# Kernel optimization log

Hardware: AMD Instinct MI355X
Metric: run time of the kernel (lower is better)

The kernel has to match this reference:

```python
import jax, jax.numpy as jnp
import numpy as np

TOP_K = 8  # num_experts_per_tok
NEG_INF = -1e9


def setup_inputs() -> dict:
    key = jax.random.key(0)
    ks = jax.random.split(key, 6)
    B, S, H, I, E, G, GS = 1, 2048, 2048, 1408, 64, 8, 8
    sc = 0.02
    return {
        "hidden_states": jax.random.normal(ks[0], (B, S, H), jnp.float32),
        "gate_w": jax.random.normal(ks[1], (E, H), jnp.float32) * sc,
        "mask_up_w": jax.random.normal(ks[2], (G, H, GS), jnp.float32) * sc,
        "gate_proj_w": jax.random.normal(ks[3], (G, I, H), jnp.float32) * sc,
        "up_proj_w": jax.random.normal(ks[4], (G, I, H), jnp.float32) * sc,
        "down_proj_w": jax.random.normal(ks[5], (G, H, I), jnp.float32) * sc,
        "inv_map": jnp.arange(G * GS, dtype=jnp.int64).reshape(G, GS),
    }


def reference(hidden_states, gate_w, mask_up_w, gate_proj_w, up_proj_w, down_proj_w, inv_map):
    B, S, H = hidden_states.shape
    x = hidden_states.reshape(-1, H)  # [N, H]
    N = x.shape[0]
    E = gate_w.shape[0]

    # Gate: softmax scores -> top-k routing (DeepSeek-style MoEGate)
    scores = jax.nn.softmax(x @ gate_w.T, axis=-1)          # [N, E]
    topk_w, topk_idx = jax.lax.top_k(scores, TOP_K)         # [N, K]

    # Per-expert routing weight: w_e[t, e] = sum_k topk_w[t,k] * (topk_idx[t,k]==e)
    w_e = jnp.zeros((N, E), x.dtype).at[jnp.arange(N)[:, None], topk_idx].add(topk_w)

    # Gather group-local weights: flat[t, g, i] for sub-expert i of group g
    flat = w_e[:, inv_map]                                   # [N, G, GS]
    scalar = flat.sum(-1)                                    # [N, G]
    soft = jax.nn.softmax(jnp.where(flat == 0, NEG_INF, flat), axis=-1)  # [N, G, GS]

    # Mask injection: x' = x + mask_up_proj(soft)
    xg = x[:, None, :] + jnp.einsum('ngi,ghi->ngh', soft, mask_up_w)     # [N, G, H]

    # SwiGLU per group
    g = jnp.einsum('ngh,gih->ngi', xg, gate_proj_w)          # [N, G, I]
    u = jnp.einsum('ngh,gih->ngi', xg, up_proj_w)            # [N, G, I]
    a = jax.nn.silu(g) * u
    d = jnp.einsum('ngi,ghi->ngh', a, down_proj_w)           # [N, G, H]

    # scalar * output, accumulated over groups (scalar==0 rows contribute 0,
    # matching the original's zero-masked scatter)
    y = jnp.einsum('ng,ngh->nh', scalar, d)
    return y.reshape(B, S, H)
```

## Files before the change

### kernel.cpp

```cpp
#include <hip/hip_runtime.h>

#define N_TOK 2048
#define H_DIM 2048
#define I_DIM 1408
#define E_EXP 64
#define G_GRP 8
#define KTOT  (G_GRP * I_DIM)
#define NQ    (G_GRP * I_DIM * H_DIM / 4)
#define NQB   (NQ / 256)

typedef __bf16 bf16x8 __attribute__((ext_vector_type(8)));
typedef float f32x4 __attribute__((ext_vector_type(4)));

__device__ __forceinline__ unsigned short f2bf(float f) {
    unsigned int u = __builtin_bit_cast(unsigned int, f);
    u += 0x7fffu + ((u >> 16) & 1u);
    return (unsigned short)(u >> 16);
}

__device__ __forceinline__ void gl_lds16(const void* g, void* l) {
    __builtin_amdgcn_global_load_lds(
        (const __attribute__((address_space(1))) unsigned int*)g,
        (__attribute__((address_space(3))) unsigned int*)l, 16, 0, 0);
}

__device__ __forceinline__ bf16x8 lds_frag(const unsigned short* sm, int row, int c) {
    return *(const bf16x8*)&sm[(row * 8 + (c ^ (row & 7))) * 8];
}

__device__ __forceinline__ bf16x8 frag32(const unsigned short* sm, int region, int row, int q) {
    return *(const bf16x8*)&sm[(region + row * 4 + (q ^ (row & 3))) * 8];
}

__global__ __launch_bounds__(256) void k_prep(const float* __restrict__ gw,
                                              const float* __restrict__ wgp,
                                              const float* __restrict__ wup,
                                              const float* __restrict__ wdp,
                                              float* __restrict__ gwT,
                                              unsigned short* __restrict__ wgB,
                                              unsigned short* __restrict__ wuB,
                                              unsigned short* __restrict__ wdB) {
    int b = blockIdx.x, t = threadIdx.x;
    if (b < 2 * NQB) {
        const float* in = (b < NQB) ? wgp : wup;
        unsigned short* out = (b < NQB) ? wgB : wuB;
        int i = (b < NQB ? b : b - NQB) * 256 + t;
        float4 v = ((const float4*)in)[i];
        ushort4 o;
        o.x = f2bf(v.x); o.y = f2bf(v.y); o.z = f2bf(v.z); o.w = f2bf(v.w);
        ((ushort4*)out)[i] = o;
    } else if (b < 3 * NQB) {
        int idx = (b - 2 * NQB) * 256 + t;
        int i4 = idx % (I_DIM / 4);
        int h  = (idx / (I_DIM / 4)) & (H_DIM - 1);
        int g  = idx / ((I_DIM / 4) * H_DIM);
        float4 v = ((const float4*)(wdp + ((size_t)g * H_DIM + h) * I_DIM))[i4];
        ushort4 o;
        o.x = f2bf(v.x); o.y = f2bf(v.y); o.z = f2bf(v.z); o.w = f2bf(v.w);
        ((ushort4*)(wdB + ((size_t)h * G_GRP + g) * I_DIM))[i4] = o;
    } else {
        int i = (b - 3 * NQB) * 256 + t;
        gwT[i] = gw[(i & 63) * H_DIM + (i >> 6)];
    }
}

__global__ __launch_bounds__(512) void k_gating(const float* __restrict__ x,
                                                const float* __restrict__ gwT,
                                                float* __restrict__ soft,
                                                float* __restrict__ scal) {
    __shared__ double smAcc[8][8][64];
    int t = threadIdx.x, wid = t >> 6, lane = t & 63;
    int n0 = blockIdx.x * 8;

    double acc[8];
#pragma unroll
    for (int k = 0; k < 8; ++k) acc[k] = 0.0;
    int h0 = wid * 256;
    for (int h = h0; h < h0 + 256; ++h) {
        float gv = gwT[h * 64 + lane];
#pragma unroll
        for (int tok = 0; tok < 8; ++tok)
            acc[tok] += (double)x[(size_t)(n0 + tok) * H_DIM + h] * (double)gv;
    }
#pragma unroll
    for (int tok = 0; tok < 8; ++tok) smAcc[wid][tok][lane] = acc[tok];
    __syncthreads();

    double lg = 0.0;
#pragma unroll
    for (int w2 = 0; w2 < 8; ++w2) lg += smAcc[w2][wid][lane];
    float logit = (float)lg;

    float mx = logit;
#pragma unroll
    for (int d = 1; d < 64; d <<= 1) mx = fmaxf(mx, __shfl_xor(mx, d));
    float ex = expf(logit - mx);
    float sm = ex;
#pragma unroll
    for (int d = 1; d < 64; d <<= 1) sm += __shfl_xor(sm, d);
    float prob = ex / sm;

    float cur = prob, w = 0.0f;
#pragma unroll
    for (int it = 0; it < 8; ++it) {
        float m = cur;
#pragma unroll
        for (int d = 1; d < 64; d <<= 1) m = fmaxf(m, __shfl_xor(m, d));
        unsigned long long msk = __ballot(cur == m);
        int first = __ffsll(msk) - 1;
        if (lane == first) { w = prob; cur = -1.0f; }
    }
    float wf = w;

    float s8 = wf;
#pragma unroll
    for (int d = 1; d < 8; d <<= 1) s8 += __shfl_xor(s8, d);
    float v = (wf == 0.0f) ? -1000000000.0f : wf;
    float m8 = v;
#pragma unroll
    for (int d = 1; d < 8; d <<= 1) m8 = fmaxf(m8, __shfl_xor(m8, d));
    float e8 = expf(v - m8);
    float q8 = e8;
#pragma unroll
    for (int d = 1; d < 8; d <<= 1) q8 += __shfl_xor(q8, d);

    int n = n0 + wid;
    soft[(size_t)n * 64 + lane] = e8 / q8;
    if ((lane & 7) == 0) scal[(size_t)n * 8 + (lane >> 3)] = s8;
}

__global__ __launch_bounds__(256) void k_xg(const float* __restrict__ x,
                                            const float* __restrict__ muw,
                                            const float* __restrict__ soft,
                                            unsigned short* __restrict__ xg) {
    int g = blockIdx.z, h0 = blockIdx.y * 1024, n0 = blockIdx.x * 128;
    __shared__ float smSf[128][8];
    int t = threadIdx.x;
    {
        int r = t >> 1, s4 = (t & 1) * 4;
        float4 sv = *(const float4*)&soft[(size_t)(n0 + r) * 64 + g * 8 + s4];
        smSf[r][s4 + 0] = sv.x; smSf[r][s4 + 1] = sv.y;
        smSf[r][s4 + 2] = sv.z; smSf[r][s4 + 3] = sv.w;
    }
    int hh = t * 4;
    float mu[8][4];
#pragma unroll
    for (int j = 0; j < 4; ++j) {
        const float4* p = (const float4*)(muw + ((size_t)g * H_DIM + h0 + hh + j) * 8);
        float4 a = p[0], b = p[1];
        mu[0][j] = a.x; mu[1][j] = a.y; mu[2][j] = a.z; mu[3][j] = a.w;
        mu[4][j] = b.x; mu[5][j] = b.y; mu[6][j] = b.z; mu[7][j] = b.w;
    }
    __syncthreads();
    for (int r = 0; r < 128; ++r) {
        float4 xv = *(const float4*)&x[(size_t)(n0 + r) * H_DIM + h0 + hh];
        float c0 = xv.x, c1 = xv.y, c2 = xv.z, c3 = xv.w;
#pragma unroll
        for (int s = 0; s < 8; ++s) {
            float w = smSf[r][s];
            c0 += w * mu[s][0]; c1 += w * mu[s][1];
            c2 += w * mu[s][2]; c3 += w * mu[s][3];
        }
        ushort4 o;
        o.x = f2bf(c0); o.y = f2bf(c1); o.z = f2bf(c2); o.w = f2bf(c3);
        *(ushort4*)&xg[((size_t)g * N_TOK + n0 + r) * H_DIM + h0 + hh] = o;
    }
}

#define NT_G1 (H_DIM / 32)

__global__ __launch_bounds__(512, 2) void k_gemm1(const unsigned short* __restrict__ xg,
                                                  const unsigned short* __restrict__ wg,
                                                  const unsigned short* __restrict__ wu,
                                                  const float* __restrict__ scal,
                                                  unsigned short* __restrict__ aB) {
    int f = blockIdx.x;
    int g = f & 7, r = f >> 3;
    int m0 = (r & 7) * 256;
    int n0 = (r >> 3) * 128;
    __shared__ __align__(16) unsigned short lds[4 * 2048 * 8];
    __shared__ float smS[256];
    int t = threadIdx.x, wid = t >> 6, lane = t & 63;
    int r16 = lane & 15, quad = lane >> 4;
    int wm = wid >> 2, wn = wid & 3;

    if (t < 256) smS[t] = scal[(size_t)(m0 + t) * 8 + g];

    const unsigned short* A  = xg + (size_t)g * N_TOK * H_DIM;
    const unsigned short* Bg = wg + (size_t)g * I_DIM * H_DIM;
    const unsigned short* Bu = wu + (size_t)g * I_DIM * H_DIM;

    int sA0 = (wid * 2 + 0) * 64 + lane;
    int sA1 = (wid * 2 + 1) * 64 + lane;
    int rA0 = sA0 >> 2, cA0 = (sA0 & 3) ^ (rA0 & 3);
    int rA1 = sA1 >> 2, cA1 = (sA1 & 3) ^ (rA1 & 3);
    int sB = wid * 64 + lane;
    int rB = sB >> 2, cB = (sB & 3) ^ (rB & 3);
    const unsigned short* gA0 = A + (size_t)(m0 + rA0) * H_DIM + cA0 * 8;
    const unsigned short* gA1 = A + (size_t)(m0 + rA1) * H_DIM + cA1 * 8;
    const unsigned short* gG  = Bg + (size_t)(n0 + rB) * H_DIM + cB * 8;
    const unsigned short* gU  = Bu + (size_t)(n0 + rB) * H_DIM + cB * 8;

#define STAGE_A(ts) do { int b_ = (ts) & 3; \
        gl_lds16(gA0 + (size_t)(ts) * 32, &lds[((size_t)b_ * 2048 + (wid * 2 + 0) * 64) * 8]); \
        gl_lds16(gA1 + (size_t)(ts) * 32, &lds[((size_t)b_ * 2048 + (wid * 2 + 1) * 64) * 8]); } while (0)
#define STAGE_GU(ts) do { int b_ = (ts) & 3; \
        gl_lds16(gG + (size_t)(ts) * 32, &lds[((size_t)b_ * 2048 + 1024 + wid * 64) * 8]); \
        gl_lds16(gU + (size_t)(ts) * 32, &lds[((size_t)b_ * 2048 + 1536 + wid * 64) * 8]); } while (0)

    f32x4 zero = {0.f, 0.f, 0.f, 0.f};
    f32x4 accg[8][2], accu[8][2];
#pragma unroll
    for (int mi = 0; mi < 8; ++mi)
#pragma unroll
        for (int ni = 0; ni < 2; ++ni) { accg[mi][ni] = zero; accu[mi][ni] = zero; }

    STAGE_A(0); STAGE_GU(0);
    STAGE_A(1); STAGE_GU(1);
    STAGE_A(2); STAGE_GU(2);
    asm volatile("s_waitcnt vmcnt(8) lgkmcnt(0)" ::: "memory");
    __builtin_amdgcn_s_barrier();

    for (int tt = 0; tt < NT_G1; ++tt) {
        const unsigned short* buf = &lds[(size_t)(tt & 3) * 2048 * 8];
        bf16x8 af[4], bgf[2], buf_[2];
#pragma unroll
        for (int mi = 0; mi < 4; ++mi)
            af[mi] = frag32(buf, 0, wm * 128 + mi * 16 + r16, quad);
#pragma unroll
        for (int ni = 0; ni < 2; ++ni) {
            bgf[ni]  = frag32(buf, 1024, wn * 32 + ni * 16 + r16, quad);
            buf_[ni] = frag32(buf, 1536, wn * 32 + ni * 16 + r16, quad);
        }
        if (tt + 3 < NT_G1) STAGE_A(tt + 3);
        __builtin_amdgcn_s_barrier();
        __builtin_amdgcn_s_setprio(1);
#pragma unroll
        for (int mi = 0; mi < 4; ++mi)
#pragma unroll
            for (int ni = 0; ni < 2; ++ni) {
                accg[mi][ni] = __builtin_amdgcn_mfma_f32_16x16x32_bf16(af[mi], bgf[ni], accg[mi][ni], 0, 0, 0);
                accu[mi][ni] = __builtin_amdgcn_mfma_f32_16x16x32_bf16(af[mi], buf_[ni], accu[mi][ni], 0, 0, 0);
            }
        __builtin_amdgcn_s_setprio(0);
        __builtin_amdgcn_s_barrier();
#pragma unroll
        for (int mi = 0; mi < 4; ++mi)
            af[mi] = frag32(buf, 0, wm * 128 + (mi + 4) * 16 + r16, quad);
        if (tt + 3 < NT_G1) STAGE_GU(tt + 3);
        __builtin_amdgcn_s_barrier();
        __builtin_amdgcn_s_setprio(1);
#pragma unroll
        for (int mi = 0; mi < 4; ++mi)
#pragma unroll
            for (int ni = 0; ni < 2; ++ni) {
                accg[mi + 4][ni] = __builtin_amdgcn_mfma_f32_16x16x32_bf16(af[mi], bgf[ni], accg[mi + 4][ni], 0, 0, 0);
                accu[mi + 4][ni] = __builtin_amdgcn_mfma_f32_16x16x32_bf16(af[mi], buf_[ni], accu[mi + 4][ni], 0, 0, 0);
            }
        __builtin_amdgcn_s_setprio(0);
        {
            int rem = NT_G1 - 2 - tt;
            if (rem >= 2)      asm volatile("s_waitcnt vmcnt(8)" ::: "memory");
            else if (rem == 1) asm volatile("s_waitcnt vmcnt(4)" ::: "memory");
            else if (rem == 0) asm volatile("s_waitcnt vmcnt(0)" ::: "memory");
        }
        __builtin_amdgcn_s_barrier();
    }
#undef STAGE_A
#undef STAGE_GU

#pragma unroll
    for (int mi = 0; mi < 8; ++mi)
#pragma unroll
        for (int ni = 0; ni < 2; ++ni)
#pragma unroll
            for (int rr = 0; rr < 4; ++rr) {
                int rl = wm * 128 + mi * 16 + quad * 4 + rr;
                int row = m0 + rl;
                int col = n0 + wn * 32 + ni * 16 + r16;
                float gv = accg[mi][ni][rr];
                float sv = gv / (1.0f + __expf(-gv));
                aB[((size_t)row * G_GRP + g) * I_DIM + col] = f2bf(sv * accu[mi][ni][rr] * smS[rl]);
            }
}

__global__ __launch_bounds__(256) void k_gemm2(const unsigned short* __restrict__ aB,
                                               const unsigned short* __restrict__ wd,
                                               float* __restrict__ out) {
    int m0 = blockIdx.x * 128, h0 = blockIdx.y * 128;
    int kbase = blockIdx.z * (KTOT / 2);
    __shared__ __align__(16) unsigned short smA[8192], smB[8192];
    int t = threadIdx.x, wid = t >> 6, lane = t & 63;
    int r16 = lane & 15, quad = lane >> 4;
    int wm = wid >> 1, wn = wid & 1;

    f32x4 zero = {0.f, 0.f, 0.f, 0.f};
    f32x4 acc[4][4];
#pragma unroll
    for (int mi = 0; mi < 4; ++mi)
#pragma unroll
        for (int ni = 0; ni < 4; ++ni) acc[mi][ni] = zero;

    for (int k0 = kbase; k0 < kbase + KTOT / 2; k0 += 64) {
#pragma unroll
        for (int j = 0; j < 4; ++j) {
            int issue = wid * 4 + j;
            int s = issue * 64 + lane;
            int row = s >> 3;
            int c = (s & 7) ^ (row & 7);
            gl_lds16(aB + (size_t)(m0 + row) * KTOT + k0 + c * 8, &smA[issue * 512]);
            gl_lds16(wd + (size_t)(h0 + row) * KTOT + k0 + c * 8, &smB[issue * 512]);
        }
        __syncthreads();
#pragma unroll
        for (int kh = 0; kh < 2; ++kh) {
            int cc = kh * 4 + quad;
            bf16x8 af[4], bf_[4];
#pragma unroll
            for (int mi = 0; mi < 4; ++mi) af[mi]  = lds_frag(smA, wm * 64 + mi * 16 + r16, cc);
#pragma unroll
            for (int ni = 0; ni < 4; ++ni) bf_[ni] = lds_frag(smB, wn * 64 + ni * 16 + r16, cc);
#pragma unroll
            for (int mi = 0; mi < 4; ++mi)
#pragma unroll
                for (int ni = 0; ni < 4; ++ni)
                    acc[mi][ni] = __builtin_amdgcn_mfma_f32_16x16x32_bf16(af[mi], bf_[ni], acc[mi][ni], 0, 0, 0);
        }
        __syncthreads();
    }

#pragma unroll
    for (int mi = 0; mi < 4; ++mi)
#pragma unroll
        for (int ni = 0; ni < 4; ++ni)
#pragma unroll
            for (int rr = 0; rr < 4; ++rr) {
                int row = m0 + wm * 64 + mi * 16 + quad * 4 + rr;
                int col = h0 + wn * 64 + ni * 16 + r16;
                atomicAdd(&out[(size_t)row * H_DIM + col], acc[mi][ni][rr]);
            }
}

extern "C" void kernel_launch(void* const* d_in, const int* in_sizes, int n_in,
                              void* d_out, int out_size, void* d_ws, size_t ws_size,
                              hipStream_t stream) {
    const float* x   = (const float*)d_in[0];
    const float* gw  = (const float*)d_in[1];
    const float* mu  = (const float*)d_in[2];
    const float* wgp = (const float*)d_in[3];
    const float* wup = (const float*)d_in[4];
    const float* wdp = (const float*)d_in[5];
    float* out = (float*)d_out;
    char* ws = (char*)d_ws;

    float* gwT  = (float*)(ws + 0);
    float* soft = (float*)(ws + 524288);
    float* scal = (float*)(ws + 1048576);
    unsigned short* wgB = (unsigned short*)(ws + 1114112);
    unsigned short* wuB = (unsigned short*)(ws + 47251456);
    unsigned short* wdB = (unsigned short*)(ws + 93388800);
    unsigned short* xg  = (unsigned short*)(ws + 139526144);
    unsigned short* aB  = (unsigned short*)(ws + 206635008);

    hipMemsetAsync(d_out, 0, (size_t)N_TOK * H_DIM * sizeof(float), stream);
    k_prep<<<3 * NQB + 512, 256, 0, stream>>>(gw, wgp, wup, wdp, gwT, wgB, wuB, wdB);
    k_gating<<<N_TOK / 8, 512, 0, stream>>>(x, gwT, soft, scal);
    k_xg<<<dim3(16, 2, 8), 256, 0, stream>>>(x, mu, soft, xg);
    k_gemm1<<<704, 512, 0, stream>>>(xg, wgB, wuB, scal, aB);
    k_gemm2<<<dim3(16, 16, 2), 256, 0, stream>>>(aB, wdB, out);
}
```

Measured before the change: 761.4 us.

## Rewrite down-projection GEMM with 256x256 tiles and 4-stage async LDS pipeline

The second GEMM moves from 128x128 tiles, 256 threads and synchronous loads with two barriers per step to 256x256 tiles with 512 threads. It now uses a four-buffer global_load_lds pipeline with staggered A/B staging and priority boosts, the same structure as the first GEMM. Split-K goes from 2 to 4, so more atomicAdds land on the output. The LDS swizzle for both GEMMs changes to a paired-row layout, which is meant to reduce bank conflicts on fragment reads.

Result: faster. 736.9 us (-3.2%).

```diff
diff --git a/kernel.cpp b/kernel.cpp
--- a/kernel.cpp
+++ b/kernel.cpp
@@ -24,12 +24,17 @@
         (__attribute__((address_space(3))) unsigned int*)l, 16, 0, 0);
 }
 
-__device__ __forceinline__ bf16x8 lds_frag(const unsigned short* sm, int row, int c) {
-    return *(const bf16x8*)&sm[(row * 8 + (c ^ (row & 7))) * 8];
-}
-
-__device__ __forceinline__ bf16x8 frag32(const unsigned short* sm, int region, int row, int q) {
-    return *(const bf16x8*)&sm[(region + row * 4 + (q ^ (row & 3))) * 8];
+__device__ __forceinline__ bf16x8 fragP(const unsigned short* sm, int region, int row, int q) {
+    int idx = region + ((row >> 1) << 3) + ((q | ((row & 1) << 2)) ^ ((row >> 1) & 7));
+    return *(const bf16x8*)&sm[idx * 8];
+}
+__device__ __forceinline__ int slot_row(int s) {
+    int line = s >> 3, u = (s & 7) ^ (line & 7);
+    return (line << 1) | (u >> 2);
+}
+__device__ __forceinline__ int slot_q(int s) {
+    int line = s >> 3, u = (s & 7) ^ (line & 7);
+    return u & 3;
 }
 
 __global__ __launch_bounds__(256) void k_prep(const float* __restrict__ gw,
@@ -192,14 +197,11 @@
 
     int sA0 = (wid * 2 + 0) * 64 + lane;
     int sA1 = (wid * 2 + 1) * 64 + lane;
-    int rA0 = sA0 >> 2, cA0 = (sA0 & 3) ^ (rA0 & 3);
-    int rA1 = sA1 >> 2, cA1 = (sA1 & 3) ^ (rA1 & 3);
-    int sB = wid * 64 + lane;
-    int rB = sB >> 2, cB = (sB & 3) ^ (rB & 3);
-    const unsigned short* gA0 = A + (size_t)(m0 + rA0) * H_DIM + cA0 * 8;
-    const unsigned short* gA1 = A + (size_t)(m0 + rA1) * H_DIM + cA1 * 8;
-    const unsigned short* gG  = Bg + (size_t)(n0 + rB) * H_DIM + cB * 8;
-    const unsigned short* gU  = Bu + (size_t)(n0 + rB) * H_DIM + cB * 8;
+    int sB  = wid * 64 + lane;
+    const unsigned short* gA0 = A + (size_t)(m0 + slot_row(sA0)) * H_DIM + slot_q(sA0) * 8;
+    const unsigned short* gA1 = A + (size_t)(m0 + slot_row(sA1)) * H_DIM + slot_q(sA1) * 8;
+    const unsigned short* gG  = Bg + (size_t)(n0 + slot_row(sB)) * H_DIM + slot_q(sB) * 8;
+    const unsigned short* gU  = Bu + (size_t)(n0 + slot_row(sB)) * H_DIM + slot_q(sB) * 8;
 
 #define STAGE_A(ts) do { int b_ = (ts) & 3; \
         gl_lds16(gA0 + (size_t)(ts) * 32, &lds[((size_t)b_ * 2048 + (wid * 2 + 0) * 64) * 8]); \
@@ -226,11 +228,11 @@
         bf16x8 af[4], bgf[2], buf_[2];
 #pragma unroll
         for (int mi = 0; mi < 4; ++mi)
-            af[mi] = frag32(buf, 0, wm * 128 + mi * 16 + r16, quad);
+            af[mi] = fragP(buf, 0, wm * 128 + mi * 16 + r16, quad);
 #pragma unroll
         for (int ni = 0; ni < 2; ++ni) {
-            bgf[ni]  = frag32(buf, 1024, wn * 32 + ni * 16 + r16, quad);
-            buf_[ni] = frag32(buf, 1536, wn * 32 + ni * 16 + r16, quad);
+            bgf[ni]  = fragP(buf, 1024, wn * 32 + ni * 16 + r16, quad);
+            buf_[ni] = fragP(buf, 1536, wn * 32 + ni * 16 + r16, quad);
         }
         if (tt + 3 < NT_G1) STAGE_A(tt + 3);
         __builtin_amdgcn_s_barrier();
@@ -246,7 +248,7 @@
         __builtin_amdgcn_s_barrier();
 #pragma unroll
         for (int mi = 0; mi < 4; ++mi)
-            af[mi] = frag32(buf, 0, wm * 128 + (mi + 4) * 16 + r16, quad);
+            af[mi] = fragP(buf, 0, wm * 128 + (mi + 4) * 16 + r16, quad);
         if (tt + 3 < NT_G1) STAGE_GU(tt + 3);
         __builtin_amdgcn_s_barrier();
         __builtin_amdgcn_s_setprio(1);
@@ -284,58 +286,94 @@
             }
 }
 
-__global__ __launch_bounds__(256) void k_gemm2(const unsigned short* __restrict__ aB,
-                                               const unsigned short* __restrict__ wd,
-                                               float* __restrict__ out) {
-    int m0 = blockIdx.x * 128, h0 = blockIdx.y * 128;
-    int kbase = blockIdx.z * (KTOT / 2);
-    __shared__ __align__(16) unsigned short smA[8192], smB[8192];
+#define NT_G2 (KTOT / 4 / 32)
+
+__global__ __launch_bounds__(512, 2) void k_gemm2(const unsigned short* __restrict__ aB,
+                                                  const unsigned short* __restrict__ wd,
+                                                  float* __restrict__ out) {
+    int m0 = blockIdx.x * 256, h0 = blockIdx.y * 256;
+    int kbase = blockIdx.z * (KTOT / 4);
+    __shared__ __align__(16) unsigned short lds[4 * 2048 * 8];
     int t = threadIdx.x, wid = t >> 6, lane = t & 63;
     int r16 = lane & 15, quad = lane >> 4;
-    int wm = wid >> 1, wn = wid & 1;
+    int wm = wid >> 2, wn = wid & 3;
+
+    int sA0 = (wid * 2 + 0) * 64 + lane;
+    int sA1 = (wid * 2 + 1) * 64 + lane;
+    const unsigned short* gA0 = aB + (size_t)(m0 + slot_row(sA0)) * KTOT + kbase + slot_q(sA0) * 8;
+    const unsigned short* gA1 = aB + (size_t)(m0 + slot_row(sA1)) * KTOT + kbase + slot_q(sA1) * 8;
+    const unsigned short* gB0 = wd + (size_t)(h0 + slot_row(sA0)) * KTOT + kbase + slot_q(sA0) * 8;
+    const unsigned short* gB1 = wd + (size_t)(h0 + slot_row(sA1)) * KTOT + kbase + slot_q(sA1) * 8;
+
+#define STAGE2A(ts) do { int b_ = (ts) & 3; \
+        gl_lds16(gA0 + (size_t)(ts) * 32, &lds[((size_t)b_ * 2048 + (wid * 2 + 0) * 64) * 8]); \
+        gl_lds16(gA1 + (size_t)(ts) * 32, &lds[((size_t)b_ * 2048 + (wid * 2 + 1) * 64) * 8]); } while (0)
+#define STAGE2B(ts) do { int b_ = (ts) & 3; \
+        gl_lds16(gB0 + (size_t)(ts) * 32, &lds[((size_t)b_ * 2048 + 1024 + (wid * 2 + 0) * 64) * 8]); \
+        gl_lds16(gB1 + (size_t)(ts) * 32, &lds[((size_t)b_ * 2048 + 1024 + (wid * 2 + 1) * 64) * 8]); } while (0)
 
     f32x4 zero = {0.f, 0.f, 0.f, 0.f};
-    f32x4 acc[4][4];
-#pragma unroll
-    for (int mi = 0; mi < 4; ++mi)
+    f32x4 acc[8][4];
+#pragma unroll
+    for (int mi = 0; mi < 8; ++mi)
 #pragma unroll
         for (int ni = 0; ni < 4; ++ni) acc[mi][ni] = zero;
 
-    for (int k0 = kbase; k0 < kbase + KTOT / 2; k0 += 64) {
-#pragma unroll
-        for (int j = 0; j < 4; ++j) {
-            int issue = wid * 4 + j;
-            int s = issue * 64 + lane;
-            int row = s >> 3;
-            int c = (s & 7) ^ (row & 7);
-            gl_lds16(aB + (size_t)(m0 + row) * KTOT + k0 + c * 8, &smA[issue * 512]);
-            gl_lds16(wd + (size_t)(h0 + row) * KTOT + k0 + c * 8, &smB[issue * 512]);
+    STAGE2A(0); STAGE2B(0);
+    STAGE2A(1); STAGE2B(1);
+    STAGE2A(2); STAGE2B(2);
+    asm volatile("s_waitcnt vmcnt(8)" ::: "memory");
+    __builtin_amdgcn_s_barrier();
+
+    for (int tt = 0; tt < NT_G2; ++tt) {
+        const unsigned short* buf = &lds[(size_t)(tt & 3) * 2048 * 8];
+        bf16x8 af[4], bf_[4];
+#pragma unroll
+        for (int mi = 0; mi < 4; ++mi)
+            af[mi] = fragP(buf, 0, wm * 128 + mi * 16 + r16, quad);
+#pragma unroll
+        for (int ni = 0; ni < 4; ++ni)
+            bf_[ni] = fragP(buf, 1024, wn * 64 + ni * 16 + r16, quad);
+        if (tt + 3 < NT_G2) STAGE2A(tt + 3);
+        __builtin_amdgcn_s_barrier();
+        __builtin_amdgcn_s_setprio(1);
+#pragma unroll
+        for (int mi = 0; mi < 4; ++mi)
+#pragma unroll
+            for (int ni = 0; ni < 4; ++ni)
+                acc[mi][ni] = __builtin_amdgcn_mfma_f32_16x16x32_bf16(af[mi], bf_[ni], acc[mi][ni], 0, 0, 0);
+        __builtin_amdgcn_s_setprio(0);
+        __builtin_amdgcn_s_barrier();
+#pragma unroll
+        for (int mi = 0; mi < 4; ++mi)
+            af[mi] = fragP(buf, 0, wm * 128 + (mi + 4) * 16 + r16, quad);
+        if (tt + 3 < NT_G2) STAGE2B(tt + 3);
+        __builtin_amdgcn_s_barrier();
+        __builtin_amdgcn_s_setprio(1);
+#pragma unroll
+        for (int mi = 0; mi < 4; ++mi)
+#pragma unroll
+            for (int ni = 0; ni < 4; ++ni)
+                acc[mi + 4][ni] = __builtin_amdgcn_mfma_f32_16x16x32_bf16(af[mi], bf_[ni], acc[mi + 4][ni], 0, 0, 0);
+        __builtin_amdgcn_s_setprio(0);
+        {
+            int rem = NT_G2 - 2 - tt;
+            if (rem >= 2)      asm volatile("s_waitcnt vmcnt(8)" ::: "memory");
+            else if (rem == 1) asm volatile("s_waitcnt vmcnt(4)" ::: "memory");
+            else if (rem == 0) asm volatile("s_waitcnt vmcnt(0)" ::: "memory");
         }
-        __syncthreads();
-#pragma unroll
-        for (int kh = 0; kh < 2; ++kh) {
-            int cc = kh * 4 + quad;
-            bf16x8 af[4], bf_[4];
-#pragma unroll
-            for (int mi = 0; mi < 4; ++mi) af[mi]  = lds_frag(smA, wm * 64 + mi * 16 + r16, cc);
-#pragma unroll
-            for (int ni = 0; ni < 4; ++ni) bf_[ni] = lds_frag(smB, wn * 64 + ni * 16 + r16, cc);
-#pragma unroll
-            for (int mi = 0; mi < 4; ++mi)
-#pragma unroll
-                for (int ni = 0; ni < 4; ++ni)
-                    acc[mi][ni] = __builtin_amdgcn_mfma_f32_16x16x32_bf16(af[mi], bf_[ni], acc[mi][ni], 0, 0, 0);
-        }
-        __syncthreads();
-    }
-
-#pragma unroll
-    for (int mi = 0; mi < 4; ++mi)
+        __builtin_amdgcn_s_barrier();
+    }
+#undef STAGE2A
+#undef STAGE2B
+
+#pragma unroll
+    for (int mi = 0; mi < 8; ++mi)
 #pragma unroll
         for (int ni = 0; ni < 4; ++ni)
 #pragma unroll
             for (int rr = 0; rr < 4; ++rr) {
-                int row = m0 + wm * 64 + mi * 16 + quad * 4 + rr;
+                int row = m0 + wm * 128 + mi * 16 + quad * 4 + rr;
                 int col = h0 + wn * 64 + ni * 16 + r16;
                 atomicAdd(&out[(size_t)row * H_DIM + col], acc[mi][ni][rr]);
             }
@@ -367,5 +405,5 @@
     k_gating<<<N_TOK / 8, 512, 0, stream>>>(x, gwT, soft, scal);
     k_xg<<<dim3(16, 2, 8), 256, 0, stream>>>(x, mu, soft, xg);
     k_gemm1<<<704, 512, 0, stream>>>(xg, wgB, wuB, scal, aB);
-    k_gemm2<<<dim3(16, 16, 2), 256, 0, stream>>>(aB, wdB, out);
-}
+    k_gemm2<<<dim3(8, 8, 4), 512, 0, stream>>>(aB, wdB, out);
+}
```
